# Optimization experiments

Hardware: AMD Instinct MI355X
Metric: run time of the kernel (lower is better)

The kernel has to match this reference:

```python
import jax, jax.numpy as jnp
import numpy as np

B, H, W, C = 1, 180, 360, 192
WS, SHIFT, NH = 6, 3, 6
MLAT, MLON = H // WS, W // WS
NW = MLAT * MLON
N = WS * WS
HD = C // NH
SCALE = HD ** -0.5
EPS = 1e-5


def _rel_index():
    # earth-specific relative position index: (MLAT, N, N) int32
    ch = np.arange(WS)
    cw = np.arange(WS)
    coords = np.stack(np.meshgrid(ch, cw, indexing='ij')).reshape(2, -1)  # (2, N)
    rel = coords[:, :, None] - coords[:, None, :]                         # (2, N, N)
    idx = (rel[0] + WS - 1) * (2 * WS - 1) + (rel[1] + WS - 1)            # (N, N)
    off = np.arange(MLAT) * (2 * WS - 1) * (2 * WS - 1)                   # per-latitude offset
    return (idx[None, :, :] + off[:, None, None]).astype(np.int32)


def _attn_mask():
    # standard shifted-window mask: (NW, N, N), 0 or -100
    img = np.zeros((H, W), dtype=np.int32)
    cnt = 0
    for hs in (slice(0, -WS), slice(-WS, -SHIFT), slice(-SHIFT, None)):
        for ws_ in (slice(0, -WS), slice(-WS, -SHIFT), slice(-SHIFT, None)):
            img[hs, ws_] = cnt
            cnt += 1
    wins = img.reshape(MLAT, WS, MLON, WS).transpose(0, 2, 1, 3).reshape(NW, N)
    diff = wins[:, None, :] - wins[:, :, None]
    return np.where(diff != 0, -100.0, 0.0).astype(np.float32)

_RPI = jnp.asarray(_rel_index())     # (MLAT, N, N)
_MASK = jnp.asarray(_attn_mask())    # (NW, N, N)


def _layernorm(x, g, b):
    mu = jnp.mean(x, axis=-1, keepdims=True)
    var = jnp.mean(jnp.square(x - mu), axis=-1, keepdims=True)
    return (x - mu) * jax.lax.rsqrt(var + EPS) * g + b


def _window_partition(x):
    # (B, H, W, C) -> (B*NW, N, C)
    x = x.reshape(B, MLAT, WS, MLON, WS, C).transpose(0, 1, 3, 2, 4, 5)
    return x.reshape(B * NW, N, C)


def _window_reverse(w):
    # (B*NW, N, C) -> (B, H, W, C)
    x = w.reshape(B, MLAT, MLON, WS, WS, C).transpose(0, 1, 3, 2, 4, 5)
    return x.reshape(B, H, W, C)


def setup_inputs() -> dict:
    key = jax.random.key(0)
    ks = jax.random.split(key, 6)
    s = 0.02
    return {
        'x': jax.random.normal(ks[0], (B, H * W, C), jnp.float32),
        'norm1_w': jnp.ones((C,), jnp.float32),
        'norm1_b': jnp.zeros((C,), jnp.float32),
        'qkv_w': jax.random.normal(ks[1], (C, 3 * C), jnp.float32) * s,
        'qkv_b': jnp.zeros((3 * C,), jnp.float32),
        'proj_w': jax.random.normal(ks[2], (C, C), jnp.float32) * s,
        'proj_b': jnp.zeros((C,), jnp.float32),
        'bias_table': jax.random.normal(ks[3], (MLAT * (2 * WS - 1) ** 2, NH), jnp.float32) * s,
        'norm2_w': jnp.ones((C,), jnp.float32),
        'norm2_b': jnp.zeros((C,), jnp.float32),
        'fc1_w': jax.random.normal(ks[4], (C, 4 * C), jnp.float32) * s,
        'fc1_b': jnp.zeros((4 * C,), jnp.float32),
        'fc2_w': jax.random.normal(ks[5], (4 * C, C), jnp.float32) * s,
        'fc2_b': jnp.zeros((C,), jnp.float32),
    }


def reference(x, norm1_w, norm1_b, qkv_w, qkv_b, proj_w, proj_b, bias_table,
              norm2_w, norm2_b, fc1_w, fc1_b, fc2_w, fc2_b):
    shortcut = x
    h = _layernorm(x, norm1_w, norm1_b).reshape(B, H, W, C)
    # cyclic shift
    h = jnp.roll(h, shift=(-SHIFT, -SHIFT), axis=(1, 2))
    xw = _window_partition(h)                                   # (B*NW, N, C)

    qkv = xw @ qkv_w + qkv_b                                    # (B_, N, 3C)
    qkv = qkv.reshape(B * NW, N, 3, NH, HD).transpose(2, 0, 3, 1, 4)
    q, k, v = qkv[0], qkv[1], qkv[2]                            # (B_, NH, N, HD)

    # earth-specific relative position bias, gathered per latitude row
    bias = jnp.take(bias_table, _RPI, axis=0)                   # (MLAT, N, N, NH)
    bias = bias.transpose(0, 3, 1, 2)[:, None]                  # (MLAT, 1, NH, N, N)
    bias = jnp.broadcast_to(bias, (MLAT, MLON, NH, N, N)).reshape(NW, NH, N, N)
    bias = bias + _MASK[:, None]                                # add shift mask

    attn = jnp.einsum('bhnd,bhmd->bhnm', q, k) * SCALE + bias
    attn = jax.nn.softmax(attn, axis=-1)
    av = jnp.einsum('bhnm,bhmd->bhnd', attn, v)                 # (B_, NH, N, HD)
    av = av.transpose(0, 2, 1, 3).reshape(B * NW, N, C)
    av = av @ proj_w + proj_b

    h = _window_reverse(av)
    h = jnp.roll(h, shift=(SHIFT, SHIFT), axis=(1, 2)).reshape(B, H * W, C)
    x = shortcut + h

    m = _layernorm(x, norm2_w, norm2_b)
    m = jax.nn.gelu(m @ fc1_w + fc1_b, approximate=False) @ fc2_w + fc2_b
    return x + m
```

## Files before the change

### kernel.cpp

```cpp
#include <hip/hip_runtime.h>
#include <hip/hip_bf16.h>

constexpr int HH   = 180;
constexpr int WW   = 360;
constexpr int CC   = 192;
constexpr int WS   = 6;
constexpr int SHIFT= 3;
constexpr int NH   = 6;
constexpr int MLAT = HH / WS;
constexpr int MLON = WW / WS;
constexpr int NWIN = MLAT * MLON;
constexpr int NTOK = WS * WS;
constexpr int HD   = CC / NH;
constexpr long M_TOK = (long)NWIN * NTOK;
constexpr long M_PAD = 65024;
constexpr float SCALE_F = 0.17677669529663687f;

typedef unsigned short ushort_t;
using bf16x8 = __attribute__((ext_vector_type(8))) short;
using f32x4  = __attribute__((ext_vector_type(4))) float;

static __device__ inline float b2f(ushort_t u) {
    union { float f; unsigned int i; } v; v.i = ((unsigned int)u) << 16; return v.f;
}
static __device__ inline ushort_t f2b(float f) {
    __hip_bfloat16 h = __float2bfloat16(f);
    return *(ushort_t*)&h;
}
static __device__ inline unsigned int cvtpk(float lo, float hi) {
    unsigned int r;
    asm("v_cvt_pk_bf16_f32 %0, %1, %2" : "=v"(r) : "v"(lo), "v"(hi));
    return r;
}

static __device__ inline void gload_lds16(const ushort_t* g, ushort_t* l) {
    __builtin_amdgcn_global_load_lds(
        (const __attribute__((address_space(1))) unsigned int*)g,
        (__attribute__((address_space(3))) unsigned int*)l, 16, 0, 0);
}

__global__ void transpose_all(const float* __restrict__ qkv_w, const float* __restrict__ proj_w,
                              const float* __restrict__ fc1_w, const float* __restrict__ fc2_w,
                              ushort_t* __restrict__ wqkv, ushort_t* __restrict__ wproj,
                              ushort_t* __restrict__ wfc1, ushort_t* __restrict__ wfc2) {
    int e = blockIdx.x * 256 + threadIdx.x;
    const float* in; ushort_t* out; int K, N;
    if (e < 110592)      { in = qkv_w;  out = wqkv;  K = 192; N = 576; }
    else if (e < 147456) { e -= 110592; in = proj_w; out = wproj; K = 192; N = 192; }
    else if (e < 294912) { e -= 147456; in = fc1_w;  out = wfc1;  K = 192; N = 768; }
    else if (e < 442368) { e -= 294912; in = fc2_w;  out = wfc2;  K = 768; N = 192; }
    else return;
    int n = e / K, k = e - n * K;
    out[e] = f2b(in[(long)k * N + n]);
}

__global__ void zero_bf16(ushort_t* __restrict__ p, int count) {
    int e = blockIdx.x * 256 + threadIdx.x;
    if (e < count) p[e] = 0;
}

static __device__ inline int region1d(int p, int L) {
    return (p < L - WS) ? 0 : ((p < L - SHIFT) ? 1 : 2);
}

__global__ void bias_mask_precompute(const float* __restrict__ bt, float* __restrict__ bm) {
    int idx = blockIdx.x * 256 + threadIdx.x;
    if (idx >= MLAT * 2 * NH * 36 * 48) return;
    int e = idx;
    int j = e % 48; e /= 48;
    int i = e % 36; e /= 36;
    int h = e % NH; e /= NH;
    int lt = e % 2;
    int mlat = e / 2;
    if (j >= 36) { bm[idx] = -1e30f; return; }
    int ih = i / WS, iw = i - ih * WS;
    int jh = j / WS, jw = j - jh * WS;
    int bidx = mlat * 121 + (ih - jh + 5) * 11 + (iw - jw + 5);
    float v = bt[bidx * NH + h];
    int mlon = lt ? (MLON - 1) : 0;
    int ri = region1d(mlat * WS + ih, HH) * 3 + region1d(mlon * WS + iw, WW);
    int rj = region1d(mlat * WS + jh, HH) * 3 + region1d(mlon * WS + jw, WW);
    if (ri != rj) v += -100.0f;
    bm[idx] = v;
}

__global__ __launch_bounds__(256) void ln1_window_kernel(
    const float* __restrict__ x, const float* __restrict__ g, const float* __restrict__ b,
    ushort_t* __restrict__ xw)
{
    long t = (long)blockIdx.x * 4 + (threadIdx.x >> 6);
    int lane = threadIdx.x & 63;
    if (t >= M_PAD) return;
    if (t >= M_TOK) {
        ushort_t* o = xw + t * CC;
        o[lane] = 0; o[lane + 64] = 0; o[lane + 128] = 0;
        return;
    }
    int ti = (int)t;
    int w = ti / NTOK, n = ti - w * NTOK;
    int mlat = w / MLON, mlon = w - mlat * MLON;
    int sh = mlat * WS + n / WS, sw = mlon * WS + (n % WS);
    int hh = sh + SHIFT; if (hh >= HH) hh -= HH;
    int ww = sw + SHIFT; if (ww >= WW) ww -= WW;
    const float* row = x + ((long)hh * WW + ww) * CC;
    float v0 = row[lane], v1 = row[lane + 64], v2 = row[lane + 128];
    float s = v0 + v1 + v2;
    float ss = v0 * v0 + v1 * v1 + v2 * v2;
    #pragma unroll
    for (int o = 32; o > 0; o >>= 1) { s += __shfl_xor(s, o, 64); ss += __shfl_xor(ss, o, 64); }
    float mu = s * (1.0f / CC);
    float var = ss * (1.0f / CC) - mu * mu;
    float rinv = rsqrtf(var + 1e-5f);
    ushort_t* o = xw + t * CC;
    o[lane]       = f2b((v0 - mu) * rinv * g[lane]       + b[lane]);
    o[lane + 64]  = f2b((v1 - mu) * rinv * g[lane + 64]  + b[lane + 64]);
    o[lane + 128] = f2b((v2 - mu) * rinv * g[lane + 128] + b[lane + 128]);
}

__global__ __launch_bounds__(256) void ln2_kernel(
    const float* __restrict__ xin, const float* __restrict__ g, const float* __restrict__ b,
    ushort_t* __restrict__ h2)
{
    long t = (long)blockIdx.x * 4 + (threadIdx.x >> 6);
    int lane = threadIdx.x & 63;
    if (t >= M_PAD) return;
    if (t >= M_TOK) {
        ushort_t* o = h2 + t * CC;
        o[lane] = 0; o[lane + 64] = 0; o[lane + 128] = 0;
        return;
    }
    const float* row = xin + t * CC;
    float v0 = row[lane], v1 = row[lane + 64], v2 = row[lane + 128];
    float s = v0 + v1 + v2;
    float ss = v0 * v0 + v1 * v1 + v2 * v2;
    #pragma unroll
    for (int o = 32; o > 0; o >>= 1) { s += __shfl_xor(s, o, 64); ss += __shfl_xor(ss, o, 64); }
    float mu = s * (1.0f / CC);
    float var = ss * (1.0f / CC) - mu * mu;
    float rinv = rsqrtf(var + 1e-5f);
    ushort_t* o = h2 + t * CC;
    o[lane]       = f2b((v0 - mu) * rinv * g[lane]       + b[lane]);
    o[lane + 64]  = f2b((v1 - mu) * rinv * g[lane + 64]  + b[lane + 64]);
    o[lane + 128] = f2b((v2 - mu) * rinv * g[lane + 128] + b[lane + 128]);
}

#define BM 128
#define BN 192
#define BK 32

template<int MODE, int KK>
__global__ __launch_bounds__(512, 3) void gemm_bf16(
    const ushort_t* __restrict__ A, const ushort_t* __restrict__ Bt,
    const float* __restrict__ bias,
    ushort_t* __restrict__ outb, float* __restrict__ outf,
    const float* __restrict__ resid,
    int N, long Mguard, int ncol, int nwg)
{
    constexpr int nk = KK / BK;
    __shared__ __align__(16) ushort_t lds[20480];
    __shared__ int row_map[BM];

    int tid = threadIdx.x;
    int lane = tid & 63;
    int wid = tid >> 6;
    int lr = lane & 15, lg = lane >> 4;
    int wm = wid >> 2, wn = wid & 3;

    int orig = blockIdx.x;
    int q = nwg >> 3, r8 = nwg & 7;
    int xcd = orig & 7, pos = orig >> 3;
    int wg = (xcd < r8 ? xcd * (q + 1) : r8 * (q + 1) + (xcd - r8) * q) + pos;
    int brow = wg / ncol, bcol = wg - brow * ncol;
    long bm0 = (long)brow * BM;
    int n0 = bcol * BN;

    if (MODE == 2 && tid < BM) {
        long t = bm0 + tid;
        if (t < M_TOK) {
            int ti = (int)t;
            int w = ti / NTOK, n = ti - w * NTOK;
            int mlat = w / MLON, mlon = w - mlat * MLON;
            int sh = mlat * WS + n / WS, sw = mlon * WS + (n % WS);
            int hh = sh + SHIFT; if (hh >= HH) hh -= HH;
            int wv = sw + SHIFT; if (wv >= WW) wv -= WW;
            row_map[tid] = hh * WW + wv;
        } else row_map[tid] = -1;
    }

    int a_pos  = tid * 16;
    int a_row  = a_pos >> 6, a_cb = a_pos & 63;
    int a_scol = (a_cb ^ ((a_row & 3) << 4)) >> 1;
    int b_row  = a_row, b_scol = a_scol;
    int b2_pos = 8192 + a_pos;
    int b2_row = b2_pos >> 6, b2_cb = b2_pos & 63;
    int b2_scol = (b2_cb ^ ((b2_row & 3) << 4)) >> 1;

#define STAGE(b, k0) do { \
    char* base = (char*)lds + (b) * 20480; \
    gload_lds16(&A[(bm0 + a_row) * KK + (k0) + a_scol], (ushort_t*)(base + a_pos)); \
    gload_lds16(&Bt[(long)(n0 + b_row) * KK + (k0) + b_scol], (ushort_t*)(base + 8192 + a_pos)); \
    if (tid < 256) \
        gload_lds16(&Bt[(long)(n0 + b2_row) * KK + (k0) + b2_scol], (ushort_t*)(base + 8192 + b2_pos)); \
} while (0)

    f32x4 acc[4][3] = {};

    STAGE(0, 0);
    asm volatile("s_waitcnt vmcnt(0)" ::: "memory");
    __builtin_amdgcn_s_barrier();

    int xr = (lr & 3) << 4;

    #pragma unroll
    for (int kt = 0; kt < nk; ++kt) {
        if (kt + 1 < nk) {
            STAGE((kt + 1) & 1, (kt + 1) * BK);
            if (wid < 4) asm volatile("s_waitcnt vmcnt(3)" ::: "memory");
            else         asm volatile("s_waitcnt vmcnt(2)" ::: "memory");
        } else {
            asm volatile("s_waitcnt vmcnt(0)" ::: "memory");
        }
        __builtin_amdgcn_s_barrier();

        const char* base = (const char*)lds + (kt & 1) * 20480;
        bf16x8 af[4], bfr[3];
        #pragma unroll
        for (int fm = 0; fm < 4; ++fm) {
            int row = wm * 64 + fm * 16 + lr;
            af[fm] = *(const bf16x8*)(base + row * 64 + ((lg * 16) ^ xr));
        }
        #pragma unroll
        for (int fn = 0; fn < 3; ++fn) {
            int row = wn * 48 + fn * 16 + lr;
            bfr[fn] = *(const bf16x8*)(base + 8192 + row * 64 + ((lg * 16) ^ xr));
        }
        __builtin_amdgcn_s_setprio(1);
        #pragma unroll
        for (int fm = 0; fm < 4; ++fm)
            #pragma unroll
            for (int fn = 0; fn < 3; ++fn)
                acc[fm][fn] = __builtin_amdgcn_mfma_f32_16x16x32_bf16(af[fm], bfr[fn], acc[fm][fn], 0, 0, 0);
        __builtin_amdgcn_s_setprio(0);
        asm volatile("s_waitcnt lgkmcnt(0)" ::: "memory");
        __builtin_amdgcn_s_barrier();
    }
#undef STAGE

    float bv[3];
    #pragma unroll
    for (int fn = 0; fn < 3; ++fn) bv[fn] = bias[n0 + wn * 48 + fn * 16 + lr];

    if (MODE == 0 || MODE == 1) {
        ushort_t* bb = lds + wid * 768;
        #pragma unroll
        for (int fm = 0; fm < 4; ++fm) {
            #pragma unroll
            for (int fn = 0; fn < 3; ++fn) {
                #pragma unroll
                for (int r = 0; r < 4; ++r) {
                    float v = acc[fm][fn][r] + bv[fn];
                    if (MODE == 0) {
                        if (n0 == 0) v *= SCALE_F;
                    }
                    if (MODE == 1) {
                        float e2 = exp2f(v * -2.4556617f);
                        v = v * __builtin_amdgcn_rcpf(1.0f + e2);
                    }
                    bb[(lg * 4 + r) * 48 + fn * 16 + lr] = f2b(v);
                }
            }
            #pragma unroll
            for (int i = 0; i < 2; ++i) {
                int cid = i * 64 + lane;
                if (cid < 96) {
                    int row = cid / 6, c6 = cid - row * 6;
                    uint4 val = *(const uint4*)&bb[row * 48 + c6 * 8];
                    long grow = bm0 + fm * 16 + row + wm * 64;
                    *(uint4*)&outb[grow * (long)N + n0 + wn * 48 + c6 * 8] = val;
                }
            }
        }
    } else {
        float* fb = (float*)lds + wid * 768;
        #pragma unroll
        for (int fm = 0; fm < 4; ++fm) {
            #pragma unroll
            for (int fn = 0; fn < 3; ++fn)
                #pragma unroll
                for (int r = 0; r < 4; ++r)
                    fb[(lg * 4 + r) * 48 + fn * 16 + lr] = acc[fm][fn][r] + bv[fn];
            #pragma unroll
            for (int i = 0; i < 3; ++i) {
                int cid = i * 64 + lane;
                int row = cid / 12, c4 = cid - row * 12;
                f32x4 val = *(const f32x4*)&fb[row * 48 + c4 * 4];
                int lrow = wm * 64 + fm * 16 + row;
                int col = wn * 48 + c4 * 4;
                if (MODE == 3) {
                    long grow = bm0 + lrow;
                    if (grow < Mguard) {
                        float* p = &outf[grow * 192 + col];
                        f32x4 old = *(const f32x4*)p;
                        *(f32x4*)p = old + val;
                    }
                } else {
                    int pp = row_map[lrow];
                    if (pp >= 0) {
                        const float* rp = &resid[(long)pp * 192 + col];
                        f32x4 rv = *(const f32x4*)rp;
                        *(f32x4*)&outf[(long)pp * 192 + col] = rv + val;
                    }
                }
            }
        }
    }
}

__global__ __launch_bounds__(256) void attn_mfma_kernel(
    const ushort_t* __restrict__ qkv,
    const float* __restrict__ bm,
    ushort_t* __restrict__ av)
{
    int wid = threadIdx.x >> 6, lane = threadIdx.x & 63;
    int unit = blockIdx.x * 4 + wid;
    int w = unit / NH, h = unit - (unit / NH) * NH;
    int mlat = w / MLON, mlon = w - mlat * MLON;
    int lr = lane & 15, lg = lane >> 4;

    const ushort_t* Qb = qkv + (long)w * NTOK * 576 + h * HD;
    const ushort_t* Kb = Qb + 192;
    const ushort_t* Vb = Qb + 384;

    bf16x8 kf[3], qf[3];
    #pragma unroll
    for (int t = 0; t < 3; ++t) {
        kf[t] = *(const bf16x8*)&Kb[(long)(t * 16 + lr) * 576 + 8 * lg];
        qf[t] = *(const bf16x8*)&Qb[(long)(t * 16 + lr) * 576 + 8 * lg];
    }
    f32x4 st[3][3] = {};
    #pragma unroll
    for (int mt = 0; mt < 3; ++mt)
        #pragma unroll
        for (int qt = 0; qt < 3; ++qt)
            st[mt][qt] = __builtin_amdgcn_mfma_f32_16x16x32_bf16(kf[mt], qf[qt], st[mt][qt], 0, 0, 0);

    bf16x8 vf[2][2];
    #pragma unroll
    for (int nd = 0; nd < 2; ++nd)
        #pragma unroll
        for (int kt = 0; kt < 2; ++kt)
            #pragma unroll
            for (int j = 0; j < 8; ++j)
                ((short*)&vf[nd][kt])[j] =
                    (short)Vb[(long)(kt * 32 + 8 * lg + j) * 576 + nd * 16 + lr];

    const float* bb = bm + (((mlat * 2 + (mlon == MLON - 1)) * NH) + h) * (36 * 48);

    f32x4 o[2][3] = {};
    int src0 = ((2 * (lg & 1)) << 4) | lr;
    int src1 = src0 + 16;

    #pragma unroll
    for (int qt = 0; qt < 3; ++qt) {
        int qrow = qt * 16 + lr;
        int qq = qrow < 36 ? qrow : 35;
        float v[3][4];
        #pragma unroll
        for (int mt = 0; mt < 3; ++mt) {
            f32x4 b4 = *(const f32x4*)&bb[qq * 48 + mt * 16 + 4 * lg];
            #pragma unroll
            for (int r = 0; r < 4; ++r) v[mt][r] = st[mt][qt][r] + b4[r];
        }
        float mx = v[0][0];
        #pragma unroll
        for (int mt = 0; mt < 3; ++mt)
            #pragma unroll
            for (int r = 0; r < 4; ++r) mx = fmaxf(mx, v[mt][r]);
        mx = fmaxf(mx, __shfl_xor(mx, 16, 64));
        mx = fmaxf(mx, __shfl_xor(mx, 32, 64));
        float p[3][4], sum = 0.f;
        #pragma unroll
        for (int mt = 0; mt < 3; ++mt)
            #pragma unroll
            for (int r = 0; r < 4; ++r) { p[mt][r] = __expf(v[mt][r] - mx); sum += p[mt][r]; }
        sum += __shfl_xor(sum, 16, 64);
        sum += __shfl_xor(sum, 32, 64);
        float rs = 1.0f / sum;

        unsigned int pk[3][2];
        #pragma unroll
        for (int mt = 0; mt < 3; ++mt) {
            pk[mt][0] = cvtpk(p[mt][0] * rs, p[mt][1] * rs);
            pk[mt][1] = cvtpk(p[mt][2] * rs, p[mt][3] * rs);
        }
        unsigned int f0[4], f1[4];
        {
            unsigned int a, b;
            a = (unsigned)__shfl((int)pk[0][0], src0, 64); b = (unsigned)__shfl((int)pk[1][0], src0, 64);
            f0[0] = (lg < 2) ? a : b;
            a = (unsigned)__shfl((int)pk[0][1], src0, 64); b = (unsigned)__shfl((int)pk[1][1], src0, 64);
            f0[1] = (lg < 2) ? a : b;
            a = (unsigned)__shfl((int)pk[0][0], src1, 64); b = (unsigned)__shfl((int)pk[1][0], src1, 64);
            f0[2] = (lg < 2) ? a : b;
            a = (unsigned)__shfl((int)pk[0][1], src1, 64); b = (unsigned)__shfl((int)pk[1][1], src1, 64);
            f0[3] = (lg < 2) ? a : b;
            f1[0] = (lg < 2) ? (unsigned)__shfl((int)pk[2][0], src0, 64) : 0u;
            f1[1] = (lg < 2) ? (unsigned)__shfl((int)pk[2][1], src0, 64) : 0u;
            f1[2] = (lg < 2) ? (unsigned)__shfl((int)pk[2][0], src1, 64) : 0u;
            f1[3] = (lg < 2) ? (unsigned)__shfl((int)pk[2][1], src1, 64) : 0u;
        }
        union { unsigned int u[4]; bf16x8 v8; } pf0, pf1;
        pf0.u[0] = f0[0]; pf0.u[1] = f0[1]; pf0.u[2] = f0[2]; pf0.u[3] = f0[3];
        pf1.u[0] = f1[0]; pf1.u[1] = f1[1]; pf1.u[2] = f1[2]; pf1.u[3] = f1[3];

        #pragma unroll
        for (int nd = 0; nd < 2; ++nd) {
            o[nd][qt] = __builtin_amdgcn_mfma_f32_16x16x32_bf16(vf[nd][0], pf0.v8, o[nd][qt], 0, 0, 0);
            o[nd][qt] = __builtin_amdgcn_mfma_f32_16x16x32_bf16(vf[nd][1], pf1.v8, o[nd][qt], 0, 0, 0);
        }
    }

    #pragma unroll
    for (int qt = 0; qt < 3; ++qt) {
        int qrow = qt * 16 + lr;
        if (qrow < NTOK) {
            #pragma unroll
            for (int nd = 0; nd < 2; ++nd) {
                uint2 pkd;
                pkd.x = cvtpk(o[nd][qt][0], o[nd][qt][1]);
                pkd.y = cvtpk(o[nd][qt][2], o[nd][qt][3]);
                *(uint2*)&av[((long)w * NTOK + qrow) * CC + h * HD + nd * 16 + 4 * lg] = pkd;
            }
        }
    }
}

extern "C" void kernel_launch(void* const* d_in, const int* in_sizes, int n_in,
                              void* d_out, int out_size, void* d_ws, size_t ws_size,
                              hipStream_t stream) {
    const float* x        = (const float*)d_in[0];
    const float* n1w      = (const float*)d_in[1];
    const float* n1b      = (const float*)d_in[2];
    const float* qkv_w    = (const float*)d_in[3];
    const float* qkv_b    = (const float*)d_in[4];
    const float* proj_w   = (const float*)d_in[5];
    const float* proj_b   = (const float*)d_in[6];
    const float* btab     = (const float*)d_in[7];
    const float* n2w      = (const float*)d_in[8];
    const float* n2b      = (const float*)d_in[9];
    const float* fc1_w    = (const float*)d_in[10];
    const float* fc1_b    = (const float*)d_in[11];
    const float* fc2_w    = (const float*)d_in[12];
    const float* fc2_b    = (const float*)d_in[13];
    float* out = (float*)d_out;

    char* p = (char*)d_ws;
    ushort_t* xw  = (ushort_t*)p;  p += M_PAD * 192 * 2;
    ushort_t* big = (ushort_t*)p;  p += M_PAD * 768 * 2;
    ushort_t* av  = (ushort_t*)p;  p += M_PAD * 192 * 2;
    ushort_t* wqkv = (ushort_t*)p; p += 576 * 192 * 2;
    ushort_t* wproj= (ushort_t*)p; p += 192 * 192 * 2;
    ushort_t* wfc1 = (ushort_t*)p; p += 768 * 192 * 2;
    ushort_t* wfc2 = (ushort_t*)p; p += 192 * 768 * 2;
    float*    bmask= (float*)p;    p += MLAT * 2 * NH * 36 * 48 * 4;

    transpose_all<<<(442368 + 255)/256, 256, 0, stream>>>(
        qkv_w, proj_w, fc1_w, fc2_w, wqkv, wproj, wfc1, wfc2);
    bias_mask_precompute<<<(MLAT*2*NH*36*48 + 255)/256, 256, 0, stream>>>(btab, bmask);
    zero_bf16<<<((int)(M_PAD - M_TOK)*192 + 255)/256, 256, 0, stream>>>(av + M_TOK * 192, (int)(M_PAD - M_TOK) * 192);

    ln1_window_kernel<<<M_PAD / 4, 256, 0, stream>>>(x, n1w, n1b, xw);

    gemm_bf16<0, 192><<<508 * 3, 512, 0, stream>>>(
        xw, wqkv, qkv_b, big, nullptr, nullptr, 576, M_PAD, 3, 508 * 3);

    attn_mfma_kernel<<<NWIN * NH / 4, 256, 0, stream>>>(big, bmask, av);

    gemm_bf16<2, 192><<<508, 512, 0, stream>>>(
        av, wproj, proj_b, nullptr, out, x, 192, M_TOK, 1, 508);

    ln2_kernel<<<M_PAD / 4, 256, 0, stream>>>(out, n2w, n2b, xw);

    gemm_bf16<1, 192><<<508 * 4, 512, 0, stream>>>(
        xw, wfc1, fc1_b, big, nullptr, nullptr, 768, M_PAD, 4, 508 * 4);

    gemm_bf16<3, 768><<<508, 512, 0, stream>>>(
        big, wfc2, fc2_b, nullptr, out, nullptr, 192, M_TOK, 1, 508);
}
```

Before: 195.5 us.

## Fuse LayerNorm2 into proj GEMM epilogue and deepen GEMM K-tile

Removes the standalone ln2 kernel. The proj GEMM epilogue now adds bias and the residual, reduces row sums and sums of squares across the four column waves through LDS, and writes both the fp32 residual output and the normalized bf16 input for fc1. This drops one kernel launch and a full re-read of the fp32 activation. Separately, the GEMM K tile grows from 32 to 64 with a larger double-buffered LDS region and an 8-row swizzle, and launch bounds are raised to 4 blocks. The larger LDS footprint and tighter register budget may cut occupancy or cause spills.

```diff
diff --git a/kernel.cpp b/kernel.cpp
--- a/kernel.cpp
+++ b/kernel.cpp
@@ -37,6 +37,15 @@
     __builtin_amdgcn_global_load_lds(
         (const __attribute__((address_space(1))) unsigned int*)g,
         (__attribute__((address_space(3))) unsigned int*)l, 16, 0, 0);
+}
+
+static __device__ inline int win_map(int ti) {
+    int w = ti / NTOK, n = ti - w * NTOK;
+    int mlat = w / MLON, mlon = w - mlat * MLON;
+    int sh = mlat * WS + n / WS, sw = mlon * WS + (n % WS);
+    int hh = sh + SHIFT; if (hh >= HH) hh -= HH;
+    int ww2 = sw + SHIFT; if (ww2 >= WW) ww2 -= WW;
+    return hh * WW + ww2;
 }
 
 __global__ void transpose_all(const float* __restrict__ qkv_w, const float* __restrict__ proj_w,
@@ -96,13 +105,8 @@
         o[lane] = 0; o[lane + 64] = 0; o[lane + 128] = 0;
         return;
     }
-    int ti = (int)t;
-    int w = ti / NTOK, n = ti - w * NTOK;
-    int mlat = w / MLON, mlon = w - mlat * MLON;
-    int sh = mlat * WS + n / WS, sw = mlon * WS + (n % WS);
-    int hh = sh + SHIFT; if (hh >= HH) hh -= HH;
-    int ww = sw + SHIFT; if (ww >= WW) ww -= WW;
-    const float* row = x + ((long)hh * WW + ww) * CC;
+    int pp = win_map((int)t);
+    const float* row = x + (long)pp * CC;
     float v0 = row[lane], v1 = row[lane + 64], v2 = row[lane + 128];
     float s = v0 + v1 + v2;
     float ss = v0 * v0 + v1 * v1 + v2 * v2;
@@ -117,48 +121,21 @@
     o[lane + 128] = f2b((v2 - mu) * rinv * g[lane + 128] + b[lane + 128]);
 }
 
-__global__ __launch_bounds__(256) void ln2_kernel(
-    const float* __restrict__ xin, const float* __restrict__ g, const float* __restrict__ b,
-    ushort_t* __restrict__ h2)
-{
-    long t = (long)blockIdx.x * 4 + (threadIdx.x >> 6);
-    int lane = threadIdx.x & 63;
-    if (t >= M_PAD) return;
-    if (t >= M_TOK) {
-        ushort_t* o = h2 + t * CC;
-        o[lane] = 0; o[lane + 64] = 0; o[lane + 128] = 0;
-        return;
-    }
-    const float* row = xin + t * CC;
-    float v0 = row[lane], v1 = row[lane + 64], v2 = row[lane + 128];
-    float s = v0 + v1 + v2;
-    float ss = v0 * v0 + v1 * v1 + v2 * v2;
-    #pragma unroll
-    for (int o = 32; o > 0; o >>= 1) { s += __shfl_xor(s, o, 64); ss += __shfl_xor(ss, o, 64); }
-    float mu = s * (1.0f / CC);
-    float var = ss * (1.0f / CC) - mu * mu;
-    float rinv = rsqrtf(var + 1e-5f);
-    ushort_t* o = h2 + t * CC;
-    o[lane]       = f2b((v0 - mu) * rinv * g[lane]       + b[lane]);
-    o[lane + 64]  = f2b((v1 - mu) * rinv * g[lane + 64]  + b[lane + 64]);
-    o[lane + 128] = f2b((v2 - mu) * rinv * g[lane + 128] + b[lane + 128]);
-}
-
 #define BM 128
 #define BN 192
-#define BK 32
+#define BK 64
 
 template<int MODE, int KK>
-__global__ __launch_bounds__(512, 3) void gemm_bf16(
+__global__ __launch_bounds__(512, 4) void gemm_bf16(
     const ushort_t* __restrict__ A, const ushort_t* __restrict__ Bt,
     const float* __restrict__ bias,
     ushort_t* __restrict__ outb, float* __restrict__ outf,
     const float* __restrict__ resid,
+    const float* __restrict__ g2, const float* __restrict__ b2,
     int N, long Mguard, int ncol, int nwg)
 {
-    constexpr int nk = KK / BK;
-    __shared__ __align__(16) ushort_t lds[20480];
-    __shared__ int row_map[BM];
+    constexpr int nt = KK / BK;
+    __shared__ __align__(16) ushort_t lds[40960];
 
     int tid = threadIdx.x;
     int lane = tid & 63;
@@ -174,33 +151,19 @@
     long bm0 = (long)brow * BM;
     int n0 = bcol * BN;
 
-    if (MODE == 2 && tid < BM) {
-        long t = bm0 + tid;
-        if (t < M_TOK) {
-            int ti = (int)t;
-            int w = ti / NTOK, n = ti - w * NTOK;
-            int mlat = w / MLON, mlon = w - mlat * MLON;
-            int sh = mlat * WS + n / WS, sw = mlon * WS + (n % WS);
-            int hh = sh + SHIFT; if (hh >= HH) hh -= HH;
-            int wv = sw + SHIFT; if (wv >= WW) wv -= WW;
-            row_map[tid] = hh * WW + wv;
-        } else row_map[tid] = -1;
-    }
-
-    int a_pos  = tid * 16;
-    int a_row  = a_pos >> 6, a_cb = a_pos & 63;
-    int a_scol = (a_cb ^ ((a_row & 3) << 4)) >> 1;
-    int b_row  = a_row, b_scol = a_scol;
-    int b2_pos = 8192 + a_pos;
-    int b2_row = b2_pos >> 6, b2_cb = b2_pos & 63;
-    int b2_scol = (b2_cb ^ ((b2_row & 3) << 4)) >> 1;
-
 #define STAGE(b, k0) do { \
-    char* base = (char*)lds + (b) * 20480; \
-    gload_lds16(&A[(bm0 + a_row) * KK + (k0) + a_scol], (ushort_t*)(base + a_pos)); \
-    gload_lds16(&Bt[(long)(n0 + b_row) * KK + (k0) + b_scol], (ushort_t*)(base + 8192 + a_pos)); \
-    if (tid < 256) \
-        gload_lds16(&Bt[(long)(n0 + b2_row) * KK + (k0) + b2_scol], (ushort_t*)(base + 8192 + b2_pos)); \
+    char* base = (char*)lds + (b) * 40960; \
+    _Pragma("unroll") \
+    for (int i = 0; i < 5; ++i) { \
+        int abs_b = tid * 16 + i * 8192; \
+        int isA = abs_b < 16384; \
+        int loc = isA ? abs_b : abs_b - 16384; \
+        int row = loc >> 7, cb = loc & 127; \
+        int scol = (cb ^ ((row & 7) << 4)) >> 1; \
+        const ushort_t* src = isA ? &A[(bm0 + row) * KK + (k0) + scol] \
+                                  : &Bt[(long)(n0 + row) * KK + (k0) + scol]; \
+        gload_lds16(src, (ushort_t*)(base + abs_b)); \
+    } \
 } while (0)
 
     f32x4 acc[4][3] = {};
@@ -209,37 +172,39 @@
     asm volatile("s_waitcnt vmcnt(0)" ::: "memory");
     __builtin_amdgcn_s_barrier();
 
-    int xr = (lr & 3) << 4;
-
-    #pragma unroll
-    for (int kt = 0; kt < nk; ++kt) {
-        if (kt + 1 < nk) {
+    int xr = (lr & 7) << 4;
+
+    #pragma unroll
+    for (int kt = 0; kt < nt; ++kt) {
+        if (kt + 1 < nt) {
             STAGE((kt + 1) & 1, (kt + 1) * BK);
-            if (wid < 4) asm volatile("s_waitcnt vmcnt(3)" ::: "memory");
-            else         asm volatile("s_waitcnt vmcnt(2)" ::: "memory");
+            asm volatile("s_waitcnt vmcnt(5)" ::: "memory");
         } else {
             asm volatile("s_waitcnt vmcnt(0)" ::: "memory");
         }
         __builtin_amdgcn_s_barrier();
 
-        const char* base = (const char*)lds + (kt & 1) * 20480;
-        bf16x8 af[4], bfr[3];
-        #pragma unroll
-        for (int fm = 0; fm < 4; ++fm) {
-            int row = wm * 64 + fm * 16 + lr;
-            af[fm] = *(const bf16x8*)(base + row * 64 + ((lg * 16) ^ xr));
-        }
-        #pragma unroll
-        for (int fn = 0; fn < 3; ++fn) {
-            int row = wn * 48 + fn * 16 + lr;
-            bfr[fn] = *(const bf16x8*)(base + 8192 + row * 64 + ((lg * 16) ^ xr));
-        }
+        const char* base = (const char*)lds + (kt & 1) * 40960;
         __builtin_amdgcn_s_setprio(1);
         #pragma unroll
-        for (int fm = 0; fm < 4; ++fm)
-            #pragma unroll
-            for (int fn = 0; fn < 3; ++fn)
-                acc[fm][fn] = __builtin_amdgcn_mfma_f32_16x16x32_bf16(af[fm], bfr[fn], acc[fm][fn], 0, 0, 0);
+        for (int s = 0; s < 2; ++s) {
+            bf16x8 af[4], bfr[3];
+            #pragma unroll
+            for (int fm = 0; fm < 4; ++fm) {
+                int row = wm * 64 + fm * 16 + lr;
+                af[fm] = *(const bf16x8*)(base + row * 128 + ((s * 64 + lg * 16) ^ xr));
+            }
+            #pragma unroll
+            for (int fn = 0; fn < 3; ++fn) {
+                int row = wn * 48 + fn * 16 + lr;
+                bfr[fn] = *(const bf16x8*)(base + 16384 + row * 128 + ((s * 64 + lg * 16) ^ xr));
+            }
+            #pragma unroll
+            for (int fm = 0; fm < 4; ++fm)
+                #pragma unroll
+                for (int fn = 0; fn < 3; ++fn)
+                    acc[fm][fn] = __builtin_amdgcn_mfma_f32_16x16x32_bf16(af[fm], bfr[fn], acc[fm][fn], 0, 0, 0);
+        }
         __builtin_amdgcn_s_setprio(0);
         asm volatile("s_waitcnt lgkmcnt(0)" ::: "memory");
         __builtin_amdgcn_s_barrier();
@@ -275,12 +240,12 @@
                 if (cid < 96) {
                     int row = cid / 6, c6 = cid - row * 6;
                     uint4 val = *(const uint4*)&bb[row * 48 + c6 * 8];
-                    long grow = bm0 + fm * 16 + row + wm * 64;
+                    long grow = bm0 + wm * 64 + fm * 16 + row;
                     *(uint4*)&outb[grow * (long)N + n0 + wn * 48 + c6 * 8] = val;
                 }
             }
         }
-    } else {
+    } else if (MODE == 3) {
         float* fb = (float*)lds + wid * 768;
         #pragma unroll
         for (int fm = 0; fm < 4; ++fm) {
@@ -294,21 +259,107 @@
                 int cid = i * 64 + lane;
                 int row = cid / 12, c4 = cid - row * 12;
                 f32x4 val = *(const f32x4*)&fb[row * 48 + c4 * 4];
-                int lrow = wm * 64 + fm * 16 + row;
+                long grow = bm0 + wm * 64 + fm * 16 + row;
                 int col = wn * 48 + c4 * 4;
-                if (MODE == 3) {
-                    long grow = bm0 + lrow;
-                    if (grow < Mguard) {
-                        float* p = &outf[grow * 192 + col];
-                        f32x4 old = *(const f32x4*)p;
-                        *(f32x4*)p = old + val;
-                    }
-                } else {
-                    int pp = row_map[lrow];
-                    if (pp >= 0) {
-                        const float* rp = &resid[(long)pp * 192 + col];
-                        f32x4 rv = *(const f32x4*)rp;
-                        *(f32x4*)&outf[(long)pp * 192 + col] = rv + val;
+                if (grow < Mguard) {
+                    float* p = &outf[grow * 192 + col];
+                    f32x4 old = *(const f32x4*)p;
+                    *(f32x4*)p = old + val;
+                }
+            }
+        }
+    } else {
+        float* redS = (float*)((char*)lds + 73728);
+        float* redQ = (float*)((char*)lds + 75776);
+        #pragma unroll
+        for (int fm = 0; fm < 4; ++fm) {
+            float s4[4], q4[4];
+            #pragma unroll
+            for (int r = 0; r < 4; ++r) {
+                int lrow = wm * 64 + fm * 16 + lg * 4 + r;
+                long t = bm0 + lrow;
+                int pp = (t < M_TOK) ? win_map((int)t) : -1;
+                float s = 0.f, qq = 0.f;
+                #pragma unroll
+                for (int fn = 0; fn < 3; ++fn) {
+                    float vv = acc[fm][fn][r] + bv[fn];
+                    if (pp >= 0) vv += resid[(long)pp * 192 + wn * 48 + fn * 16 + lr];
+                    acc[fm][fn][r] = vv;
+                    s += vv; qq += vv * vv;
+                }
+                s4[r] = s; q4[r] = qq;
+            }
+            #pragma unroll
+            for (int off = 1; off < 16; off <<= 1)
+                #pragma unroll
+                for (int r = 0; r < 4; ++r) {
+                    s4[r] += __shfl_xor(s4[r], off, 64);
+                    q4[r] += __shfl_xor(q4[r], off, 64);
+                }
+            if (lr == 0) {
+                #pragma unroll
+                for (int r = 0; r < 4; ++r) {
+                    int row = wm * 64 + fm * 16 + lg * 4 + r;
+                    redS[row * 4 + wn] = s4[r];
+                    redQ[row * 4 + wn] = q4[r];
+                }
+            }
+        }
+        asm volatile("s_waitcnt lgkmcnt(0)" ::: "memory");
+        __builtin_amdgcn_s_barrier();
+
+        float gv[3], bv2[3];
+        #pragma unroll
+        for (int fn = 0; fn < 3; ++fn) {
+            gv[fn]  = g2[wn * 48 + fn * 16 + lr];
+            bv2[fn] = b2[wn * 48 + fn * 16 + lr];
+        }
+
+        float* fb = (float*)lds + wid * 768;
+        ushort_t* bb = (ushort_t*)((char*)lds + 24576) + wid * 768;
+        #pragma unroll
+        for (int fm = 0; fm < 4; ++fm) {
+            float mu4[4], rin4[4];
+            #pragma unroll
+            for (int r = 0; r < 4; ++r) {
+                int row = wm * 64 + fm * 16 + lg * 4 + r;
+                float s = redS[row * 4 + 0] + redS[row * 4 + 1] + redS[row * 4 + 2] + redS[row * 4 + 3];
+                float qq = redQ[row * 4 + 0] + redQ[row * 4 + 1] + redQ[row * 4 + 2] + redQ[row * 4 + 3];
+                float mu = s * (1.0f / 192.0f);
+                float var = qq * (1.0f / 192.0f) - mu * mu;
+                mu4[r] = mu;
+                rin4[r] = rsqrtf(var + 1e-5f);
+            }
+            #pragma unroll
+            for (int fn = 0; fn < 3; ++fn)
+                #pragma unroll
+                for (int r = 0; r < 4; ++r) {
+                    float vv = acc[fm][fn][r];
+                    fb[(lg * 4 + r) * 48 + fn * 16 + lr] = vv;
+                    bb[(lg * 4 + r) * 48 + fn * 16 + lr] =
+                        f2b((vv - mu4[r]) * rin4[r] * gv[fn] + bv2[fn]);
+                }
+            #pragma unroll
+            for (int i = 0; i < 3; ++i) {
+                int cid = i * 64 + lane;
+                int row = cid / 12, c4 = cid - row * 12;
+                long t = bm0 + wm * 64 + fm * 16 + row;
+                if (t < M_TOK) {
+                    int pp = win_map((int)t);
+                    f32x4 val = *(const f32x4*)&fb[row * 48 + c4 * 4];
+                    *(f32x4*)&outf[(long)pp * 192 + wn * 48 + c4 * 4] = val;
+                }
+            }
+            #pragma unroll
+            for (int i = 0; i < 2; ++i) {
+                int cid = i * 64 + lane;
+                if (cid < 96) {
+                    int row = cid / 6, c6 = cid - row * 6;
+                    long t = bm0 + wm * 64 + fm * 16 + row;
+                    if (t < M_TOK) {
+                        int pp = win_map((int)t);
+                        uint4 val = *(const uint4*)&bb[row * 48 + c6 * 8];
+                        *(uint4*)&outb[(long)pp * 192 + wn * 48 + c6 * 8] = val;
                     }
                 }
             }
@@ -472,18 +523,16 @@
     ln1_window_kernel<<<M_PAD / 4, 256, 0, stream>>>(x, n1w, n1b, xw);
 
     gemm_bf16<0, 192><<<508 * 3, 512, 0, stream>>>(
-        xw, wqkv, qkv_b, big, nullptr, nullptr, 576, M_PAD, 3, 508 * 3);
+        xw, wqkv, qkv_b, big, nullptr, nullptr, nullptr, nullptr, 576, M_PAD, 3, 508 * 3);
 
     attn_mfma_kernel<<<NWIN * NH / 4, 256, 0, stream>>>(big, bmask, av);
 
     gemm_bf16<2, 192><<<508, 512, 0, stream>>>(
-        av, wproj, proj_b, nullptr, out, x, 192, M_TOK, 1, 508);
-
-    ln2_kernel<<<M_PAD / 4, 256, 0, stream>>>(out, n2w, n2b, xw);
+        av, wproj, proj_b, xw, out, x, n2w, n2b, 192, M_TOK, 1, 508);
 
     gemm_bf16<1, 192><<<508 * 4, 512, 0, stream>>>(
-        xw, wfc1, fc1_b, big, nullptr, nullptr, 768, M_PAD, 4, 508 * 4);
+        xw, wfc1, fc1_b, big, nullptr, nullptr, nullptr, nullptr, 768, M_PAD, 4, 508 * 4);
 
     gemm_bf16<3, 768><<<508, 512, 0, stream>>>(
-        big, wfc2, fc2_b, nullptr, out, nullptr, 192, M_TOK, 1, 508);
-}
+        big, wfc2, fc2_b, nullptr, out, nullptr, nullptr, nullptr, 192, M_TOK, 1, 508);
+}
```

Result: slower. 202.3 us (+3.5%).
